# Performance work log

Hardware: AMD Instinct MI355X
Metric: run time of the kernel (lower is better)

The kernel has to match this reference:

```python
import jax, jax.numpy as jnp
import numpy as np

B, T, X, H, Z, G, Y = 4096, 32, 256, 256, 256, 128, 2


def _xavier(key, fan_in, fan_out):
    lim = float(np.sqrt(6.0 / (fan_in + fan_out)))
    return jax.random.uniform(key, (fan_in, fan_out), jnp.float32, -lim, lim)


def setup_inputs() -> dict:
    key = jax.random.key(0)
    ks = jax.random.split(key, 18)
    return {
        "x": jax.random.normal(ks[0], (B, T, X), jnp.float32),
        "y_ph": jax.random.uniform(ks[1], (B, T, Y), jnp.float32),
        "T_ph": jax.random.randint(ks[2], (B,), 1, T + 1),  # 1..T valid days
        "h0": jnp.tanh(jax.random.normal(ks[3], (B, H), jnp.float32)),   # tanh(randn) init state
        "z0": jnp.tanh(jax.random.normal(ks[4], (B, Z), jnp.float32)),
        "eps": jax.random.normal(ks[5], (T, B, Z), jnp.float32),          # reparam noise per step
        # gate / candidate nets: fan_in = x + h + z
        "Wr": _xavier(ks[6], X + H + Z, H), "br": jnp.zeros((H,), jnp.float32),
        "Wu": _xavier(ks[7], X + H + Z, H), "bu": jnp.zeros((H,), jnp.float32),
        "Wh": _xavier(ks[8], X + H + Z, H), "bh": jnp.zeros((H,), jnp.float32),
        # prior latent net: fan_in = x + h
        "Wzp": _xavier(ks[9], X + H, Z), "bzp": jnp.zeros((Z,), jnp.float32),
        "Wpm": _xavier(ks[10], Z, Z), "bpm": jnp.zeros((Z,), jnp.float32),
        "Wps": _xavier(ks[11], Z, Z), "bps": jnp.zeros((Z,), jnp.float32),
        # posterior latent net: fan_in = x + h + y
        "Wzq": _xavier(ks[12], X + H + Y, Z), "bzq": jnp.zeros((Z,), jnp.float32),
        "Wqm": _xavier(ks[13], Z, Z), "bqm": jnp.zeros((Z,), jnp.float32),
        "Wqs": _xavier(ks[14], Z, Z), "bqs": jnp.zeros((Z,), jnp.float32),
        # output nets
        "Wg": _xavier(ks[15], X + H + Z, G), "bg": jnp.zeros((G,), jnp.float32),
        "Wy": _xavier(ks[16], G, Y), "by": jnp.zeros((Y,), jnp.float32),
    }


def reference(x, y_ph, T_ph, h0, z0, eps,
              Wr, br, Wu, bu, Wh, bh,
              Wzp, bzp, Wpm, bpm, Wps, bps,
              Wzq, bzq, Wqm, bqm, Wqs, bqs,
              Wg, bg, Wy, by):
    x_t = jnp.transpose(x, (1, 0, 2))     # [T, B, X]
    y_t = jnp.transpose(y_ph, (1, 0, 2))  # [T, B, Y]

    def step(carry, inp):
        h_prev, z_prev = carry
        xt, yt, et = inp
        ga = jnp.concatenate([xt, h_prev, z_prev], axis=-1)
        r = jax.nn.sigmoid(ga @ Wr + br)
        u = jax.nn.sigmoid(ga @ Wu + bu)
        ha = jnp.concatenate([xt, r * h_prev, z_prev], axis=-1)
        h_tilde = jnp.tanh(ha @ Wh + bh)
        h = (1.0 - u) * h_prev + u * h_tilde
        # prior p(z_t | x_t, h_t): z_prior = mean (is_prior=True)
        hzp = jnp.tanh(jnp.concatenate([xt, h], axis=-1) @ Wzp + bzp)
        mu_p = hzp @ Wpm + bpm
        sd_p = jnp.sqrt(jnp.exp(hzp @ Wps + bps))
        z_prior = mu_p
        # posterior q(z_t | x_t, h_t, y_t): reparameterized sample
        hzq = jnp.tanh(jnp.concatenate([xt, h, yt], axis=-1) @ Wzq + bzq)
        mu_q = hzq @ Wqm + bqm
        sd_q = jnp.sqrt(jnp.exp(hzq @ Wqs + bqs))
        z_post = mu_q + sd_q * et
        # KL(q || p) for diagonal Normals
        kl = jnp.log(sd_p / sd_q) + (sd_q ** 2 + (mu_q - mu_p) ** 2) / (2.0 * sd_p ** 2) - 0.5
        return (h, z_post), (h, z_post, z_prior, kl)

    (_, _), (h_s, z_post, z_prior, kl) = jax.lax.scan(step, (h0, z0), (x_t, y_t, eps))
    h_s = jnp.transpose(h_s, (1, 0, 2))      # [B, T, H]
    z_post = jnp.transpose(z_post, (1, 0, 2))
    kl = jnp.transpose(kl, (1, 0, 2)).sum(axis=-1)  # [B, T]

    g = jnp.tanh(jnp.concatenate([x, h_s, z_post], axis=-1) @ Wg + bg)  # [B, T, G]
    y = jax.nn.softmax(g @ Wy + by, axis=-1)                             # [B, T, Y]
    g_T = g[jnp.arange(x.shape[0]), T_ph - 1]                            # [B, G] (training, daily_att)
    return (y, kl, g_T)
```

## Files before the change

### kernel.cpp

```cpp
#include <hip/hip_runtime.h>

typedef unsigned short u16;
typedef unsigned int u32;
typedef __attribute__((ext_vector_type(8))) short short8;
typedef __attribute__((ext_vector_type(4))) float float4v;

#define B_SZ 4096
#define T_SZ 32
#define XD 256
#define HD 256
#define ZD 256
#define GD 128
#define YD 2

#define BM 32
#define NW 16

#define W1_OFF 0
#define W2_OFF 393216
#define W3_OFF 589824
#define W4_OFF 868352
#define WG_OFF 1130496
#define WTOT   1228800

#define YTOT  (B_SZ*T_SZ*YD)
#define KLTOT (B_SZ*T_SZ)

#define HST 260
#define UST 264

__device__ __forceinline__ u16 f2bf(float f) {
    u32 u = __float_as_uint(f);
    u32 r = (u + 0x7fffu + ((u >> 16) & 1u)) >> 16;
    return (u16)r;
}
__device__ __forceinline__ float bf2f(u16 h) {
    return __uint_as_float(((u32)h) << 16);
}
__device__ __forceinline__ float tanh_f(float x) {
    float e = __expf(2.f * x);
    return 1.f - 2.f / (e + 1.f);
}
__device__ __forceinline__ float sigm_f(float x) {
    return 1.f / (1.f + __expf(-x));
}

__device__ __forceinline__ int aga_off(int r, int k) {
    return (((r >> 4) * 24 + (k >> 5)) << 9) + ((((k >> 3) & 3) * 16 + (r & 15)) << 3) + (k & 7);
}
__device__ __forceinline__ int a3s_off(int r, int k, int pq) {
    return (((pq * 2 + (r >> 4)) * 8 + (k >> 5)) << 9) + ((((k >> 3) & 3) * 16 + (r & 15)) << 3) + (k & 7);
}

#define MFMA(a, b, c) __builtin_amdgcn_mfma_f32_16x16x32_bf16(a, b, c, 0, 0, 0)

__global__ void prep_weights(const float* __restrict__ Wr, const float* __restrict__ Wu,
                             const float* __restrict__ Wh, const float* __restrict__ Wzp,
                             const float* __restrict__ Wzq, const float* __restrict__ Wpm,
                             const float* __restrict__ Wps, const float* __restrict__ Wqm,
                             const float* __restrict__ Wqs, const float* __restrict__ Wg,
                             u16* __restrict__ wts)
{
    int o = blockIdx.x * 256 + threadIdx.x;
    if (o >= WTOT) return;
    int mat, w, KT;
    if (o < W2_OFF)      { mat = 0; w = o;          KT = 24; }
    else if (o < W3_OFF) { mat = 1; w = o - W2_OFF; KT = 24; }
    else if (o < W4_OFF) { mat = 2; w = o - W3_OFF; KT = 17; }
    else if (o < WG_OFF) { mat = 3; w = o - W4_OFF; KT = 8;  }
    else                 { mat = 4; w = o - WG_OFF; KT = 24; }
    int nt  = w / (KT * 512);
    int rem = w - nt * (KT * 512);
    int kt  = rem >> 9;
    int q   = rem & 511;
    int lane = q >> 3, j = q & 7;
    int n = (nt << 4) | (lane & 15);
    int k = (kt << 5) + ((lane >> 4) << 3) + j;
    float v = 0.f;
    switch (mat) {
        case 0: v = (n < 256) ? Wr[k * 256 + n] : Wu[k * 256 + (n - 256)]; break;
        case 1: v = Wh[k * 256 + n]; break;
        case 2: v = (n < 256) ? (k < 512 ? Wzp[k * 256 + n] : 0.f)
                              : (k < 514 ? Wzq[k * 256 + (n - 256)] : 0.f); break;
        case 3: { int sel = n >> 8; int nn = n & 255;
                  const float* s = (sel == 0) ? Wpm : (sel == 1) ? Wps : (sel == 2) ? Wqm : Wqs;
                  v = s[k * 256 + nn]; } break;
        default: v = Wg[k * 128 + n]; break;
    }
    wts[o] = f2bf(v);
}

__global__ __launch_bounds__(1024, 4) void vrnn_all(
    const float* __restrict__ x,   const float* __restrict__ y_ph,
    const int*   __restrict__ Tph, const float* __restrict__ h0,
    const float* __restrict__ z0,  const float* __restrict__ eps,
    const float* __restrict__ br,  const float* __restrict__ bu,
    const float* __restrict__ bh,  const float* __restrict__ bzp,
    const float* __restrict__ bpm, const float* __restrict__ bps,
    const float* __restrict__ bzq, const float* __restrict__ bqm,
    const float* __restrict__ bqs, const float* __restrict__ bg,
    const float* __restrict__ by,  const float* __restrict__ Wy,
    const u16*   __restrict__ wts, float* __restrict__ out)
{
    __shared__ __align__(16) u16   a_ga[48 * 512];
    __shared__ __align__(16) u16   a3s[32 * 512];
    __shared__ __align__(16) float h32[BM * HST];
    __shared__ __align__(16) u16   u_bf[BM * UST];
    __shared__ float part[8 * BM * 2];
    __shared__ float kl_acc[BM];
    __shared__ int   tph_s[BM];

    const int tid  = threadIdx.x;
    const int wv   = tid >> 6;
    const int lane = tid & 63;
    const int quad = lane >> 4;
    const int l15  = lane & 15;
    const int b0   = blockIdx.x * BM;

    const int c10 = wv * 32 + l15;
    const float bs1_0 = (c10 < 256) ? br[c10] : bu[c10 - 256];
    const float bs1_1 = (c10 + 16 < 256) ? br[c10 + 16] : bu[c10 + 16 - 256];
    const int c2  = wv * 16 + l15;
    const float bh_r = bh[c2];
    const float bz0 = (c10 < 256) ? bzp[c10] : bzq[c10 - 256];
    const float bz1 = (c10 + 16 < 256) ? bzp[c10 + 16] : bzq[c10 + 16 - 256];
    const int zc  = wv * 16 + l15;
    const float b4pm = bpm[zc], b4ps = bps[zc], b4qm = bqm[zc], b4qs = bqs[zc];
    const int c5  = (wv >> 1) * 16 + l15;
    const int mt5 = wv & 1;
    const float bg_r = bg[c5];
    const float wy0 = Wy[c5 * 2], wy1 = Wy[c5 * 2 + 1];
    const float by0 = by[0], by1 = by[1];

    if (tid < BM) tph_s[tid] = Tph[b0 + tid];

    {
        int r = tid >> 5, cc = (tid & 31) * 8;
        const float* hp = &h0[(b0 + r) * HD + cc];
        const float* zp = &z0[(b0 + r) * ZD + cc];
        short8 hv, zv;
#pragma unroll
        for (int j = 0; j < 8; ++j) {
            float hh = hp[j];
            h32[r * HST + cc + j] = hh;
            hv[j] = (short)f2bf(hh);
            zv[j] = (short)f2bf(zp[j]);
        }
        *(short8*)&a_ga[aga_off(r, 256 + cc)] = hv;
        *(short8*)&a_ga[aga_off(r, 512 + cc)] = zv;
    }
    __syncthreads();

    const float4v zero4 = {0.f, 0.f, 0.f, 0.f};

    for (int t = 0; t < T_SZ; ++t) {
        {
            int r = tid >> 5, cc = (tid & 31) * 8;
            const float* xp = &x[((size_t)(b0 + r) * T_SZ + t) * XD + cc];
            short8 xv;
#pragma unroll
            for (int j = 0; j < 8; ++j) xv[j] = (short)f2bf(xp[j]);
            *(short8*)&a_ga[aga_off(r, cc)] = xv;
        }
        __syncthreads();

        {
            const u16* pB0 = wts + W1_OFF + (((wv * 2    ) * 24) << 9) + lane * 8;
            const u16* pB1 = wts + W1_OFF + (((wv * 2 + 1) * 24) << 9) + lane * 8;
            float4v a00 = zero4, a01 = zero4, a10 = zero4, a11 = zero4;
            short8 b0c = *(const short8*)pB0;
            short8 b1c = *(const short8*)pB1;
            for (int kt = 0; kt < 24; ++kt) {
                int kn = (kt < 23) ? kt + 1 : 23;
                short8 b0n = *(const short8*)(pB0 + (kn << 9));
                short8 b1n = *(const short8*)(pB1 + (kn << 9));
                short8 aF0 = *(const short8*)&a_ga[(kt << 9) + lane * 8];
                short8 aF1 = *(const short8*)&a_ga[((24 + kt) << 9) + lane * 8];
                a00 = MFMA(aF0, b0c, a00); a01 = MFMA(aF0, b1c, a01);
                a10 = MFMA(aF1, b0c, a10); a11 = MFMA(aF1, b1c, a11);
                b0c = b0n; b1c = b1n;
            }
            __syncthreads();
#pragma unroll
            for (int mt = 0; mt < 2; ++mt) {
                const float4v* am = (mt == 0) ? &a00 : &a10;
                const float4v* an = (mt == 0) ? &a01 : &a11;
#pragma unroll
                for (int i = 0; i < 4; ++i) {
                    int row = mt * 16 + quad * 4 + i;
                    {
                        int c = c10;
                        float v = (*am)[i];
                        if (c < 256) {
                            float rr = sigm_f(v + bs1_0);
                            a_ga[aga_off(row, 256 + c)] = f2bf(rr * h32[row * HST + c]);
                        } else {
                            u_bf[row * UST + (c - 256)] = f2bf(sigm_f(v + bs1_0));
                        }
                    }
                    {
                        int c = c10 + 16;
                        float v = (*an)[i];
                        if (c < 256) {
                            float rr = sigm_f(v + bs1_1);
                            a_ga[aga_off(row, 256 + c)] = f2bf(rr * h32[row * HST + c]);
                        } else {
                            u_bf[row * UST + (c - 256)] = f2bf(sigm_f(v + bs1_1));
                        }
                    }
                }
            }
            __syncthreads();
        }

        {
            const u16* pB = wts + W2_OFF + ((wv * 24) << 9) + lane * 8;
            float4v a0 = zero4, a1 = zero4;
            short8 bc = *(const short8*)pB;
            for (int kt = 0; kt < 24; ++kt) {
                int kn = (kt < 23) ? kt + 1 : 23;
                short8 bn = *(const short8*)(pB + (kn << 9));
                short8 aF0 = *(const short8*)&a_ga[(kt << 9) + lane * 8];
                short8 aF1 = *(const short8*)&a_ga[((24 + kt) << 9) + lane * 8];
                a0 = MFMA(aF0, bc, a0);
                a1 = MFMA(aF1, bc, a1);
                bc = bn;
            }
            __syncthreads();
#pragma unroll
            for (int mt = 0; mt < 2; ++mt) {
                const float4v* am = (mt == 0) ? &a0 : &a1;
#pragma unroll
                for (int i = 0; i < 4; ++i) {
                    int row = mt * 16 + quad * 4 + i;
                    float ht = tanh_f((*am)[i] + bh_r);
                    float uu = bf2f(u_bf[row * UST + c2]);
                    float hp = h32[row * HST + c2];
                    float h  = (1.f - uu) * hp + uu * ht;
                    h32[row * HST + c2] = h;
                    a_ga[aga_off(row, 256 + c2)] = f2bf(h);
                }
            }
            if (tid < 128) {
                int r = tid >> 2, grp = tid & 3;
                short8 v = {0, 0, 0, 0, 0, 0, 0, 0};
                if (grp == 0) {
                    const float* yp = &y_ph[((size_t)(b0 + r) * T_SZ + t) * YD];
                    v[0] = (short)f2bf(yp[0]);
                    v[1] = (short)f2bf(yp[1]);
                }
                *(short8*)&a_ga[aga_off(r, 512 + grp * 8)] = v;
            }
            __syncthreads();
        }

        {
            const u16* pB0 = wts + W3_OFF + (((wv * 2    ) * 17) << 9) + lane * 8;
            const u16* pB1 = wts + W3_OFF + (((wv * 2 + 1) * 17) << 9) + lane * 8;
            float4v a00 = zero4, a01 = zero4, a10 = zero4, a11 = zero4;
            short8 b0c = *(const short8*)pB0;
            short8 b1c = *(const short8*)pB1;
            for (int kt = 0; kt < 17; ++kt) {
                int kn = (kt < 16) ? kt + 1 : 16;
                short8 b0n = *(const short8*)(pB0 + (kn << 9));
                short8 b1n = *(const short8*)(pB1 + (kn << 9));
                short8 aF0 = *(const short8*)&a_ga[(kt << 9) + lane * 8];
                short8 aF1 = *(const short8*)&a_ga[((24 + kt) << 9) + lane * 8];
                a00 = MFMA(aF0, b0c, a00); a01 = MFMA(aF0, b1c, a01);
                a10 = MFMA(aF1, b0c, a10); a11 = MFMA(aF1, b1c, a11);
                b0c = b0n; b1c = b1n;
            }
#pragma unroll
            for (int mt = 0; mt < 2; ++mt) {
                const float4v* am = (mt == 0) ? &a00 : &a10;
                const float4v* an = (mt == 0) ? &a01 : &a11;
#pragma unroll
                for (int i = 0; i < 4; ++i) {
                    int row = mt * 16 + quad * 4 + i;
                    {
                        int c = c10;
                        float hz = tanh_f((*am)[i] + bz0);
                        a3s[a3s_off(row, c & 255, c >> 8)] = f2bf(hz);
                    }
                    {
                        int c = c10 + 16;
                        float hz = tanh_f((*an)[i] + bz1);
                        a3s[a3s_off(row, c & 255, c >> 8)] = f2bf(hz);
                    }
                }
            }
            if (tid < BM) kl_acc[tid] = 0.f;
            __syncthreads();
        }

        {
            const u16* pB0 = wts + W4_OFF + (((0 * 16 + wv) * 8) << 9) + lane * 8;
            const u16* pB1 = wts + W4_OFF + (((1 * 16 + wv) * 8) << 9) + lane * 8;
            const u16* pB2 = wts + W4_OFF + (((2 * 16 + wv) * 8) << 9) + lane * 8;
            const u16* pB3 = wts + W4_OFF + (((3 * 16 + wv) * 8) << 9) + lane * 8;
            float4v ac[4][2];
#pragma unroll
            for (int m = 0; m < 4; ++m) { ac[m][0] = zero4; ac[m][1] = zero4; }
            for (int kt = 0; kt < 8; ++kt) {
                short8 bm0 = *(const short8*)(pB0 + (kt << 9));
                short8 bm1 = *(const short8*)(pB1 + (kt << 9));
                short8 bm2 = *(const short8*)(pB2 + (kt << 9));
                short8 bm3 = *(const short8*)(pB3 + (kt << 9));
                short8 aP0 = *(const short8*)&a3s[((0 + kt) << 9) + lane * 8];
                short8 aP1 = *(const short8*)&a3s[((8 + kt) << 9) + lane * 8];
                short8 aQ0 = *(const short8*)&a3s[((16 + kt) << 9) + lane * 8];
                short8 aQ1 = *(const short8*)&a3s[((24 + kt) << 9) + lane * 8];
                ac[0][0] = MFMA(aP0, bm0, ac[0][0]); ac[0][1] = MFMA(aP1, bm0, ac[0][1]);
                ac[1][0] = MFMA(aP0, bm1, ac[1][0]); ac[1][1] = MFMA(aP1, bm1, ac[1][1]);
                ac[2][0] = MFMA(aQ0, bm2, ac[2][0]); ac[2][1] = MFMA(aQ1, bm2, ac[2][1]);
                ac[3][0] = MFMA(aQ0, bm3, ac[3][0]); ac[3][1] = MFMA(aQ1, bm3, ac[3][1]);
            }
            float kls[2][4];
#pragma unroll
            for (int mt = 0; mt < 2; ++mt)
#pragma unroll
                for (int i = 0; i < 4; ++i) {
                    int row = mt * 16 + quad * 4 + i;
                    float mu_p = ac[0][mt][i] + b4pm;
                    float s_p  = ac[1][mt][i] + b4ps;
                    float mu_q = ac[2][mt][i] + b4qm;
                    float s_q  = ac[3][mt][i] + b4qs;
                    float e = eps[((size_t)t * B_SZ + (b0 + row)) * ZD + zc];
                    float zpost = mu_q + __expf(0.5f * s_q) * e;
                    float dmu = mu_q - mu_p;
                    kls[mt][i] = 0.5f * (s_p - s_q)
                               + (__expf(s_q) + dmu * dmu) * 0.5f * __expf(-s_p) - 0.5f;
                    a_ga[aga_off(row, 512 + zc)] = f2bf(zpost);
                }
#pragma unroll
            for (int mt = 0; mt < 2; ++mt)
#pragma unroll
                for (int i = 0; i < 4; ++i) {
                    float v = kls[mt][i];
                    v += __shfl_xor(v, 1); v += __shfl_xor(v, 2);
                    v += __shfl_xor(v, 4); v += __shfl_xor(v, 8);
                    if (l15 == 0) atomicAdd(&kl_acc[mt * 16 + quad * 4 + i], v);
                }
            __syncthreads();
            if (tid < BM)
                out[YTOT + (size_t)(b0 + tid) * T_SZ + t] = kl_acc[tid];
        }

        {
            const u16* pB = wts + WG_OFF + (((wv >> 1) * 24) << 9) + lane * 8;
            float4v a5 = zero4;
            short8 bc = *(const short8*)pB;
            const int abase = mt5 * 24;
            for (int kt = 0; kt < 24; ++kt) {
                int kn = (kt < 23) ? kt + 1 : 23;
                short8 bn = *(const short8*)(pB + (kn << 9));
                short8 aF = *(const short8*)&a_ga[((abase + kt) << 9) + lane * 8];
                a5 = MFMA(aF, bc, a5);
                bc = bn;
            }
            float g[4];
#pragma unroll
            for (int i = 0; i < 4; ++i) {
                int row = mt5 * 16 + quad * 4 + i;
                g[i] = tanh_f(a5[i] + bg_r);
                if (tph_s[row] - 1 == t)
                    out[YTOT + KLTOT + (size_t)(b0 + row) * GD + c5] = g[i];
            }
#pragma unroll
            for (int i = 0; i < 4; ++i) {
                float p0 = g[i] * wy0, p1 = g[i] * wy1;
                p0 += __shfl_xor(p0, 1); p0 += __shfl_xor(p0, 2);
                p0 += __shfl_xor(p0, 4); p0 += __shfl_xor(p0, 8);
                p1 += __shfl_xor(p1, 1); p1 += __shfl_xor(p1, 2);
                p1 += __shfl_xor(p1, 4); p1 += __shfl_xor(p1, 8);
                if (l15 == 0) {
                    int row = mt5 * 16 + quad * 4 + i;
                    part[((wv >> 1) * BM + row) * 2]     = p0;
                    part[((wv >> 1) * BM + row) * 2 + 1] = p1;
                }
            }
            __syncthreads();
            if (tid < BM) {
                int r = tid;
                float s0 = by0, s1 = by1;
#pragma unroll
                for (int j = 0; j < 8; ++j) {
                    s0 += part[(j * BM + r) * 2];
                    s1 += part[(j * BM + r) * 2 + 1];
                }
                float mx = fmaxf(s0, s1);
                float e0 = __expf(s0 - mx), e1 = __expf(s1 - mx);
                float inv = 1.f / (e0 + e1);
                size_t yoff = ((size_t)(b0 + r) * T_SZ + t) * YD;
                out[yoff]     = e0 * inv;
                out[yoff + 1] = e1 * inv;
            }
        }
    }
}

extern "C" void kernel_launch(void* const* d_in, const int* in_sizes, int n_in,
                              void* d_out, int out_size, void* d_ws, size_t ws_size,
                              hipStream_t stream)
{
    const float* x   = (const float*)d_in[0];
    const float* yph = (const float*)d_in[1];
    const int*   Tph = (const int*)  d_in[2];
    const float* h0  = (const float*)d_in[3];
    const float* z0  = (const float*)d_in[4];
    const float* eps = (const float*)d_in[5];
    const float* Wr  = (const float*)d_in[6];
    const float* br  = (const float*)d_in[7];
    const float* Wu  = (const float*)d_in[8];
    const float* bu  = (const float*)d_in[9];
    const float* Wh  = (const float*)d_in[10];
    const float* bh  = (const float*)d_in[11];
    const float* Wzp = (const float*)d_in[12];
    const float* bzp = (const float*)d_in[13];
    const float* Wpm = (const float*)d_in[14];
    const float* bpm = (const float*)d_in[15];
    const float* Wps = (const float*)d_in[16];
    const float* bps = (const float*)d_in[17];
    const float* Wzq = (const float*)d_in[18];
    const float* bzq = (const float*)d_in[19];
    const float* Wqm = (const float*)d_in[20];
    const float* bqm = (const float*)d_in[21];
    const float* Wqs = (const float*)d_in[22];
    const float* bqs = (const float*)d_in[23];
    const float* Wg  = (const float*)d_in[24];
    const float* bg  = (const float*)d_in[25];
    const float* Wy  = (const float*)d_in[26];
    const float* by  = (const float*)d_in[27];
    u16*   wts = (u16*)d_ws;
    float* out = (float*)d_out;

    hipLaunchKernelGGL(prep_weights, dim3((WTOT + 255) / 256), dim3(256), 0, stream,
                       Wr, Wu, Wh, Wzp, Wzq, Wpm, Wps, Wqm, Wqs, Wg, wts);
    hipLaunchKernelGGL(vrnn_all, dim3(B_SZ / BM), dim3(1024), 0, stream,
                       x, yph, Tph, h0, z0, eps, br, bu, bh, bzp, bpm, bps,
                       bzq, bqm, bqs, bg, by, Wy, wts, out);
}
```

Baseline: 4.635 ms.

## Keep GRU state in registers, deepen weight prefetch, add grid barrier per step

```diff
diff --git a/kernel.cpp b/kernel.cpp
--- a/kernel.cpp
+++ b/kernel.cpp
@@ -14,7 +14,7 @@
 #define YD 2
 
 #define BM 32
-#define NW 16
+#define NBLK (B_SZ / BM)
 
 #define W1_OFF 0
 #define W2_OFF 393216
@@ -26,16 +26,10 @@
 #define YTOT  (B_SZ*T_SZ*YD)
 #define KLTOT (B_SZ*T_SZ)
 
-#define HST 260
-#define UST 264
-
 __device__ __forceinline__ u16 f2bf(float f) {
     u32 u = __float_as_uint(f);
     u32 r = (u + 0x7fffu + ((u >> 16) & 1u)) >> 16;
     return (u16)r;
-}
-__device__ __forceinline__ float bf2f(u16 h) {
-    return __uint_as_float(((u32)h) << 16);
 }
 __device__ __forceinline__ float tanh_f(float x) {
     float e = __expf(2.f * x);
@@ -59,9 +53,10 @@
                              const float* __restrict__ Wzq, const float* __restrict__ Wpm,
                              const float* __restrict__ Wps, const float* __restrict__ Wqm,
                              const float* __restrict__ Wqs, const float* __restrict__ Wg,
-                             u16* __restrict__ wts)
+                             u16* __restrict__ wts, u32* __restrict__ bar)
 {
     int o = blockIdx.x * 256 + threadIdx.x;
+    if (o == 0) *bar = 0;
     if (o >= WTOT) return;
     int mat, w, KT;
     if (o < W2_OFF)      { mat = 0; w = o;          KT = 24; }
@@ -100,12 +95,11 @@
     const float* __restrict__ bzq, const float* __restrict__ bqm,
     const float* __restrict__ bqs, const float* __restrict__ bg,
     const float* __restrict__ by,  const float* __restrict__ Wy,
-    const u16*   __restrict__ wts, float* __restrict__ out)
+    const u16*   __restrict__ wts, u32* __restrict__ bar,
+    float* __restrict__ out)
 {
     __shared__ __align__(16) u16   a_ga[48 * 512];
     __shared__ __align__(16) u16   a3s[32 * 512];
-    __shared__ __align__(16) float h32[BM * HST];
-    __shared__ __align__(16) u16   u_bf[BM * UST];
     __shared__ float part[8 * BM * 2];
     __shared__ float kl_acc[BM];
     __shared__ int   tph_s[BM];
@@ -116,16 +110,11 @@
     const int quad = lane >> 4;
     const int l15  = lane & 15;
     const int b0   = blockIdx.x * BM;
-
-    const int c10 = wv * 32 + l15;
-    const float bs1_0 = (c10 < 256) ? br[c10] : bu[c10 - 256];
-    const float bs1_1 = (c10 + 16 < 256) ? br[c10 + 16] : bu[c10 + 16 - 256];
-    const int c2  = wv * 16 + l15;
-    const float bh_r = bh[c2];
-    const float bz0 = (c10 < 256) ? bzp[c10] : bzq[c10 - 256];
-    const float bz1 = (c10 + 16 < 256) ? bzp[c10 + 16] : bzq[c10 + 16 - 256];
-    const int zc  = wv * 16 + l15;
-    const float b4pm = bpm[zc], b4ps = bps[zc], b4qm = bqm[zc], b4qs = bqs[zc];
+    const int cst  = wv * 16 + l15;
+
+    const float br_r  = br[cst],  bu_r = bu[cst], bh_r = bh[cst];
+    const float bzp_r = bzp[cst], bzq_r = bzq[cst];
+    const float b4pm = bpm[cst], b4ps = bps[cst], b4qm = bqm[cst], b4qs = bqs[cst];
     const int c5  = (wv >> 1) * 16 + l15;
     const int mt5 = wv & 1;
     const float bg_r = bg[c5];
@@ -134,6 +123,13 @@
 
     if (tid < BM) tph_s[tid] = Tph[b0 + tid];
 
+    float h_reg[2][4];
+    float u_reg[2][4];
+#pragma unroll
+    for (int mt = 0; mt < 2; ++mt)
+#pragma unroll
+        for (int i = 0; i < 4; ++i)
+            h_reg[mt][i] = h0[(size_t)(b0 + mt * 16 + quad * 4 + i) * HD + cst];
     {
         int r = tid >> 5, cc = (tid & 31) * 8;
         const float* hp = &h0[(b0 + r) * HD + cc];
@@ -141,9 +137,7 @@
         short8 hv, zv;
 #pragma unroll
         for (int j = 0; j < 8; ++j) {
-            float hh = hp[j];
-            h32[r * HST + cc + j] = hh;
-            hv[j] = (short)f2bf(hh);
+            hv[j] = (short)f2bf(hp[j]);
             zv[j] = (short)f2bf(zp[j]);
         }
         *(short8*)&a_ga[aga_off(r, 256 + cc)] = hv;
@@ -165,49 +159,39 @@
         __syncthreads();
 
         {
-            const u16* pB0 = wts + W1_OFF + (((wv * 2    ) * 24) << 9) + lane * 8;
-            const u16* pB1 = wts + W1_OFF + (((wv * 2 + 1) * 24) << 9) + lane * 8;
-            float4v a00 = zero4, a01 = zero4, a10 = zero4, a11 = zero4;
-            short8 b0c = *(const short8*)pB0;
-            short8 b1c = *(const short8*)pB1;
+            const u16* pB0 = wts + W1_OFF + ((wv * 24) << 9) + lane * 8;
+            const u16* pB1 = wts + W1_OFF + (((16 + wv) * 24) << 9) + lane * 8;
+            short8 b0p[3], b1p[3];
+#pragma unroll
+            for (int d = 0; d < 3; ++d) {
+                b0p[d] = *(const short8*)(pB0 + (d << 9));
+                b1p[d] = *(const short8*)(pB1 + (d << 9));
+            }
+            float4v aR0 = zero4, aR1 = zero4, aU0 = zero4, aU1 = zero4;
+#pragma unroll
             for (int kt = 0; kt < 24; ++kt) {
-                int kn = (kt < 23) ? kt + 1 : 23;
-                short8 b0n = *(const short8*)(pB0 + (kn << 9));
-                short8 b1n = *(const short8*)(pB1 + (kn << 9));
+                short8 b0c = b0p[kt % 3];
+                short8 b1c = b1p[kt % 3];
+                if (kt + 3 < 24) {
+                    b0p[kt % 3] = *(const short8*)(pB0 + ((kt + 3) << 9));
+                    b1p[kt % 3] = *(const short8*)(pB1 + ((kt + 3) << 9));
+                }
                 short8 aF0 = *(const short8*)&a_ga[(kt << 9) + lane * 8];
                 short8 aF1 = *(const short8*)&a_ga[((24 + kt) << 9) + lane * 8];
-                a00 = MFMA(aF0, b0c, a00); a01 = MFMA(aF0, b1c, a01);
-                a10 = MFMA(aF1, b0c, a10); a11 = MFMA(aF1, b1c, a11);
-                b0c = b0n; b1c = b1n;
+                aR0 = MFMA(aF0, b0c, aR0); aR1 = MFMA(aF1, b0c, aR1);
+                aU0 = MFMA(aF0, b1c, aU0); aU1 = MFMA(aF1, b1c, aU1);
             }
             __syncthreads();
 #pragma unroll
             for (int mt = 0; mt < 2; ++mt) {
-                const float4v* am = (mt == 0) ? &a00 : &a10;
-                const float4v* an = (mt == 0) ? &a01 : &a11;
+                float4v vR = (mt == 0) ? aR0 : aR1;
+                float4v vU = (mt == 0) ? aU0 : aU1;
 #pragma unroll
                 for (int i = 0; i < 4; ++i) {
                     int row = mt * 16 + quad * 4 + i;
-                    {
-                        int c = c10;
-                        float v = (*am)[i];
-                        if (c < 256) {
-                            float rr = sigm_f(v + bs1_0);
-                            a_ga[aga_off(row, 256 + c)] = f2bf(rr * h32[row * HST + c]);
-                        } else {
-                            u_bf[row * UST + (c - 256)] = f2bf(sigm_f(v + bs1_0));
-                        }
-                    }
-                    {
-                        int c = c10 + 16;
-                        float v = (*an)[i];
-                        if (c < 256) {
-                            float rr = sigm_f(v + bs1_1);
-                            a_ga[aga_off(row, 256 + c)] = f2bf(rr * h32[row * HST + c]);
-                        } else {
-                            u_bf[row * UST + (c - 256)] = f2bf(sigm_f(v + bs1_1));
-                        }
-                    }
+                    float rr = sigm_f(vR[i] + br_r);
+                    u_reg[mt][i] = sigm_f(vU[i] + bu_r);
+                    a_ga[aga_off(row, 256 + cst)] = f2bf(rr * h_reg[mt][i]);
                 }
             }
             __syncthreads();
@@ -215,30 +199,31 @@
 
         {
             const u16* pB = wts + W2_OFF + ((wv * 24) << 9) + lane * 8;
+            short8 bp[3];
+#pragma unroll
+            for (int d = 0; d < 3; ++d) bp[d] = *(const short8*)(pB + (d << 9));
             float4v a0 = zero4, a1 = zero4;
-            short8 bc = *(const short8*)pB;
+#pragma unroll
             for (int kt = 0; kt < 24; ++kt) {
-                int kn = (kt < 23) ? kt + 1 : 23;
-                short8 bn = *(const short8*)(pB + (kn << 9));
+                short8 bc = bp[kt % 3];
+                if (kt + 3 < 24) bp[kt % 3] = *(const short8*)(pB + ((kt + 3) << 9));
                 short8 aF0 = *(const short8*)&a_ga[(kt << 9) + lane * 8];
                 short8 aF1 = *(const short8*)&a_ga[((24 + kt) << 9) + lane * 8];
                 a0 = MFMA(aF0, bc, a0);
                 a1 = MFMA(aF1, bc, a1);
-                bc = bn;
             }
             __syncthreads();
 #pragma unroll
             for (int mt = 0; mt < 2; ++mt) {
-                const float4v* am = (mt == 0) ? &a0 : &a1;
+                float4v va = (mt == 0) ? a0 : a1;
 #pragma unroll
                 for (int i = 0; i < 4; ++i) {
                     int row = mt * 16 + quad * 4 + i;
-                    float ht = tanh_f((*am)[i] + bh_r);
-                    float uu = bf2f(u_bf[row * UST + c2]);
-                    float hp = h32[row * HST + c2];
-                    float h  = (1.f - uu) * hp + uu * ht;
-                    h32[row * HST + c2] = h;
-                    a_ga[aga_off(row, 256 + c2)] = f2bf(h);
+                    float ht = tanh_f(va[i] + bh_r);
+                    float uu = u_reg[mt][i];
+                    float h  = (1.f - uu) * h_reg[mt][i] + uu * ht;
+                    h_reg[mt][i] = h;
+                    a_ga[aga_off(row, 256 + cst)] = f2bf(h);
                 }
             }
             if (tid < 128) {
@@ -255,38 +240,37 @@
         }
 
         {
-            const u16* pB0 = wts + W3_OFF + (((wv * 2    ) * 17) << 9) + lane * 8;
-            const u16* pB1 = wts + W3_OFF + (((wv * 2 + 1) * 17) << 9) + lane * 8;
-            float4v a00 = zero4, a01 = zero4, a10 = zero4, a11 = zero4;
-            short8 b0c = *(const short8*)pB0;
-            short8 b1c = *(const short8*)pB1;
+            const u16* pB0 = wts + W3_OFF + ((wv * 17) << 9) + lane * 8;
+            const u16* pB1 = wts + W3_OFF + (((16 + wv) * 17) << 9) + lane * 8;
+            short8 b0p[3], b1p[3];
+#pragma unroll
+            for (int d = 0; d < 3; ++d) {
+                b0p[d] = *(const short8*)(pB0 + (d << 9));
+                b1p[d] = *(const short8*)(pB1 + (d << 9));
+            }
+            float4v aP0 = zero4, aP1 = zero4, aQ0 = zero4, aQ1 = zero4;
+#pragma unroll
             for (int kt = 0; kt < 17; ++kt) {
-                int kn = (kt < 16) ? kt + 1 : 16;
-                short8 b0n = *(const short8*)(pB0 + (kn << 9));
-                short8 b1n = *(const short8*)(pB1 + (kn << 9));
+                short8 b0c = b0p[kt % 3];
+                short8 b1c = b1p[kt % 3];
+                if (kt + 3 < 17) {
+                    b0p[kt % 3] = *(const short8*)(pB0 + ((kt + 3) << 9));
+                    b1p[kt % 3] = *(const short8*)(pB1 + ((kt + 3) << 9));
+                }
                 short8 aF0 = *(const short8*)&a_ga[(kt << 9) + lane * 8];
                 short8 aF1 = *(const short8*)&a_ga[((24 + kt) << 9) + lane * 8];
-                a00 = MFMA(aF0, b0c, a00); a01 = MFMA(aF0, b1c, a01);
-                a10 = MFMA(aF1, b0c, a10); a11 = MFMA(aF1, b1c, a11);
-                b0c = b0n; b1c = b1n;
+                aP0 = MFMA(aF0, b0c, aP0); aP1 = MFMA(aF1, b0c, aP1);
+                aQ0 = MFMA(aF0, b1c, aQ0); aQ1 = MFMA(aF1, b1c, aQ1);
             }
 #pragma unroll
             for (int mt = 0; mt < 2; ++mt) {
-                const float4v* am = (mt == 0) ? &a00 : &a10;
-                const float4v* an = (mt == 0) ? &a01 : &a11;
+                float4v vP = (mt == 0) ? aP0 : aP1;
+                float4v vQ = (mt == 0) ? aQ0 : aQ1;
 #pragma unroll
                 for (int i = 0; i < 4; ++i) {
                     int row = mt * 16 + quad * 4 + i;
-                    {
-                        int c = c10;
-                        float hz = tanh_f((*am)[i] + bz0);
-                        a3s[a3s_off(row, c & 255, c >> 8)] = f2bf(hz);
-                    }
-                    {
-                        int c = c10 + 16;
-                        float hz = tanh_f((*an)[i] + bz1);
-                        a3s[a3s_off(row, c & 255, c >> 8)] = f2bf(hz);
-                    }
+                    a3s[a3s_off(row, cst, 0)] = f2bf(tanh_f(vP[i] + bzp_r));
+                    a3s[a3s_off(row, cst, 1)] = f2bf(tanh_f(vQ[i] + bzq_r));
                 }
             }
             if (tid < BM) kl_acc[tid] = 0.f;
@@ -294,26 +278,42 @@
         }
 
         {
-            const u16* pB0 = wts + W4_OFF + (((0 * 16 + wv) * 8) << 9) + lane * 8;
-            const u16* pB1 = wts + W4_OFF + (((1 * 16 + wv) * 8) << 9) + lane * 8;
-            const u16* pB2 = wts + W4_OFF + (((2 * 16 + wv) * 8) << 9) + lane * 8;
-            const u16* pB3 = wts + W4_OFF + (((3 * 16 + wv) * 8) << 9) + lane * 8;
+            float eps_r[2][4];
+#pragma unroll
+            for (int mt = 0; mt < 2; ++mt)
+#pragma unroll
+                for (int i = 0; i < 4; ++i) {
+                    int row = mt * 16 + quad * 4 + i;
+                    eps_r[mt][i] = eps[((size_t)t * B_SZ + (b0 + row)) * ZD + cst];
+                }
+            const u16* pW = wts + W4_OFF + ((wv * 8) << 9) + lane * 8;
+            const int selstr = (128 << 9);
             float4v ac[4][2];
 #pragma unroll
             for (int m = 0; m < 4; ++m) { ac[m][0] = zero4; ac[m][1] = zero4; }
+            short8 cur[4];
+#pragma unroll
+            for (int s = 0; s < 4; ++s) cur[s] = *(const short8*)(pW + s * selstr);
+#pragma unroll
             for (int kt = 0; kt < 8; ++kt) {
-                short8 bm0 = *(const short8*)(pB0 + (kt << 9));
-                short8 bm1 = *(const short8*)(pB1 + (kt << 9));
-                short8 bm2 = *(const short8*)(pB2 + (kt << 9));
-                short8 bm3 = *(const short8*)(pB3 + (kt << 9));
+                short8 nxt[4];
+                if (kt + 1 < 8) {
+#pragma unroll
+                    for (int s = 0; s < 4; ++s)
+                        nxt[s] = *(const short8*)(pW + s * selstr + ((kt + 1) << 9));
+                }
                 short8 aP0 = *(const short8*)&a3s[((0 + kt) << 9) + lane * 8];
                 short8 aP1 = *(const short8*)&a3s[((8 + kt) << 9) + lane * 8];
                 short8 aQ0 = *(const short8*)&a3s[((16 + kt) << 9) + lane * 8];
                 short8 aQ1 = *(const short8*)&a3s[((24 + kt) << 9) + lane * 8];
-                ac[0][0] = MFMA(aP0, bm0, ac[0][0]); ac[0][1] = MFMA(aP1, bm0, ac[0][1]);
-                ac[1][0] = MFMA(aP0, bm1, ac[1][0]); ac[1][1] = MFMA(aP1, bm1, ac[1][1]);
-                ac[2][0] = MFMA(aQ0, bm2, ac[2][0]); ac[2][1] = MFMA(aQ1, bm2, ac[2][1]);
-                ac[3][0] = MFMA(aQ0, bm3, ac[3][0]); ac[3][1] = MFMA(aQ1, bm3, ac[3][1]);
+                ac[0][0] = MFMA(aP0, cur[0], ac[0][0]); ac[0][1] = MFMA(aP1, cur[0], ac[0][1]);
+                ac[1][0] = MFMA(aP0, cur[1], ac[1][0]); ac[1][1] = MFMA(aP1, cur[1], ac[1][1]);
+                ac[2][0] = MFMA(aQ0, cur[2], ac[2][0]); ac[2][1] = MFMA(aQ1, cur[2], ac[2][1]);
+                ac[3][0] = MFMA(aQ0, cur[3], ac[3][0]); ac[3][1] = MFMA(aQ1, cur[3], ac[3][1]);
+                if (kt + 1 < 8) {
+#pragma unroll
+                    for (int s = 0; s < 4; ++s) cur[s] = nxt[s];
+                }
             }
             float kls[2][4];
 #pragma unroll
@@ -325,12 +325,11 @@
                     float s_p  = ac[1][mt][i] + b4ps;
                     float mu_q = ac[2][mt][i] + b4qm;
                     float s_q  = ac[3][mt][i] + b4qs;
-                    float e = eps[((size_t)t * B_SZ + (b0 + row)) * ZD + zc];
-                    float zpost = mu_q + __expf(0.5f * s_q) * e;
+                    float zpost = mu_q + __expf(0.5f * s_q) * eps_r[mt][i];
                     float dmu = mu_q - mu_p;
                     kls[mt][i] = 0.5f * (s_p - s_q)
                                + (__expf(s_q) + dmu * dmu) * 0.5f * __expf(-s_p) - 0.5f;
-                    a_ga[aga_off(row, 512 + zc)] = f2bf(zpost);
+                    a_ga[aga_off(row, 512 + cst)] = f2bf(zpost);
                 }
 #pragma unroll
             for (int mt = 0; mt < 2; ++mt)
@@ -348,15 +347,17 @@
 
         {
             const u16* pB = wts + WG_OFF + (((wv >> 1) * 24) << 9) + lane * 8;
+            short8 bp[3];
+#pragma unroll
+            for (int d = 0; d < 3; ++d) bp[d] = *(const short8*)(pB + (d << 9));
             float4v a5 = zero4;
-            short8 bc = *(const short8*)pB;
             const int abase = mt5 * 24;
+#pragma unroll
             for (int kt = 0; kt < 24; ++kt) {
-                int kn = (kt < 23) ? kt + 1 : 23;
-                short8 bn = *(const short8*)(pB + (kn << 9));
+                short8 bc = bp[kt % 3];
+                if (kt + 3 < 24) bp[kt % 3] = *(const short8*)(pB + ((kt + 3) << 9));
                 short8 aF = *(const short8*)&a_ga[((abase + kt) << 9) + lane * 8];
                 a5 = MFMA(aF, bc, a5);
-                bc = bn;
             }
             float g[4];
 #pragma unroll
@@ -395,6 +396,21 @@
                 out[yoff]     = e0 * inv;
                 out[yoff + 1] = e1 * inv;
             }
+        }
+
+        if (t + 1 < T_SZ) {
+            __syncthreads();
+            if (tid == 0) {
+                __hip_atomic_fetch_add(bar, 1u, __ATOMIC_RELAXED, __HIP_MEMORY_SCOPE_AGENT);
+                u32 target = (u32)NBLK * (u32)(t + 1);
+                int guard = 0;
+                while (__hip_atomic_load(bar, __ATOMIC_RELAXED, __HIP_MEMORY_SCOPE_AGENT) < target
+                       && guard < (1 << 22)) {
+                    __builtin_amdgcn_s_sleep(2);
+                    ++guard;
+                }
+            }
+            __syncthreads();
         }
     }
 }
@@ -431,12 +447,13 @@
     const float* bg  = (const float*)d_in[25];
     const float* Wy  = (const float*)d_in[26];
     const float* by  = (const float*)d_in[27];
-    u16*   wts = (u16*)d_ws;
+    u16* wts = (u16*)d_ws;
+    u32* bar = (u32*)((char*)d_ws + (size_t)WTOT * 2);
     float* out = (float*)d_out;
 
     hipLaunchKernelGGL(prep_weights, dim3((WTOT + 255) / 256), dim3(256), 0, stream,
-                       Wr, Wu, Wh, Wzp, Wzq, Wpm, Wps, Wqm, Wqs, Wg, wts);
-    hipLaunchKernelGGL(vrnn_all, dim3(B_SZ / BM), dim3(1024), 0, stream,
+                       Wr, Wu, Wh, Wzp, Wzq, Wpm, Wps, Wqm, Wqs, Wg, wts, bar);
+    hipLaunchKernelGGL(vrnn_all, dim3(NBLK), dim3(1024), 0, stream,
                        x, yph, Tph, h0, z0, eps, br, bu, bh, bzp, bpm, bps,
-                       bzq, bqm, bqs, bg, by, Wy, wts, out);
-}
+                       bzq, bqm, bqs, bg, by, Wy, wts, bar, out);
+}
```

After: 4.964 ms. +7.1%, slower.
